# Performance work log

Measured on AMD Instinct MI355X. Metric: run time of the kernel, lower is better.

## Reference

```python
import jax, jax.numpy as jnp
import numpy as np

N, IN_C, HID, OUT_C, DEPTH = 4096, 128, 256, 128, 3
KS = [2048, 1024, 512]  # ceil(0.5 * N_level)
E = 131072


def glorot(key, fan_in, fan_out):
    lim = np.sqrt(6.0 / (fan_in + fan_out))
    return jax.random.uniform(key, (fan_in, fan_out), jnp.float32, -lim, lim)


def build_adj(edge_index, n):
    # symmetric, self-loop-free adjacency with unit edge weights
    A = jnp.zeros((n, n), jnp.float32)
    A = A.at[edge_index[0], edge_index[1]].set(1.0)
    A = jnp.maximum(A, A.T)
    return A * (1.0 - jnp.eye(n, dtype=jnp.float32))


def gcn(x, A, W, b):
    # GCNConv(improved=True): A_hat = A + 2I, symmetric normalization
    n = A.shape[0]
    Ah = A + 2.0 * jnp.eye(n, dtype=A.dtype)
    deg = Ah.sum(axis=1)
    dinv = jnp.where(deg > 0, deg ** -0.5, 0.0)
    An = dinv[:, None] * Ah * dinv[None, :]
    return An @ (x @ W) + b


def augment(A):
    # remove self loops, add self loops (w=1), square (spspmm), remove self loops
    n = A.shape[0]
    I = jnp.eye(n, dtype=A.dtype)
    Al = A * (1.0 - I) + I
    A2 = Al @ Al
    return A2 * (1.0 - I)


def topk_pool(x, A, p, k):
    score = jnp.tanh((x @ p) / jnp.linalg.norm(p))
    vals, perm = jax.lax.top_k(score, k)
    return x[perm] * vals[:, None], A[perm][:, perm], perm


def setup_inputs() -> dict:
    key = jax.random.key(0)
    ks = jax.random.split(key, 16)
    x = jax.random.normal(ks[0], (N, IN_C), jnp.float32)
    edge_index = jax.random.randint(ks[1], (2, E), 0, N, jnp.int32)
    d = {"x": x, "edge_index": edge_index}
    d["Wd0"], d["bd0"] = glorot(ks[2], IN_C, HID), jnp.zeros((HID,), jnp.float32)
    d["Wd1"], d["bd1"] = glorot(ks[3], HID, HID), jnp.zeros((HID,), jnp.float32)
    d["Wd2"], d["bd2"] = glorot(ks[4], HID, HID), jnp.zeros((HID,), jnp.float32)
    d["Wd3"], d["bd3"] = glorot(ks[5], HID, HID), jnp.zeros((HID,), jnp.float32)
    d["p1"] = jax.random.normal(ks[6], (HID,), jnp.float32)
    d["p2"] = jax.random.normal(ks[7], (HID,), jnp.float32)
    d["p3"] = jax.random.normal(ks[8], (HID,), jnp.float32)
    d["Wu0"], d["bu0"] = glorot(ks[9], HID, HID), jnp.zeros((HID,), jnp.float32)
    d["Wu1"], d["bu1"] = glorot(ks[10], HID, HID), jnp.zeros((HID,), jnp.float32)
    d["Wu2"], d["bu2"] = glorot(ks[11], HID, OUT_C), jnp.zeros((OUT_C,), jnp.float32)
    return d


def reference(x, edge_index, Wd0, bd0, Wd1, bd1, Wd2, bd2, Wd3, bd3,
              p1, p2, p3, Wu0, bu0, Wu1, bu1, Wu2, bu2):
    n = x.shape[0]
    A = build_adj(edge_index, n)
    x = jax.nn.relu(gcn(x, A, Wd0, bd0))
    xs, As, perms = [x], [A], []
    down = [(Wd1, bd1), (Wd2, bd2), (Wd3, bd3)]
    pools = [p1, p2, p3]
    for i in range(DEPTH):
        A = augment(A)
        x, A, perm = topk_pool(x, A, pools[i], KS[i])
        x = jax.nn.relu(gcn(x, A, *down[i]))
        if i < DEPTH - 1:
            xs.append(x)
            As.append(A)
        perms.append(perm)
    up = [(Wu0, bu0), (Wu1, bu1), (Wu2, bu2)]
    for i in range(DEPTH):
        j = DEPTH - 1 - i
        res, perm = xs[j], perms[j]
        u = jnp.zeros_like(res).at[perm].set(x)
        x = res + u  # sum_res=True
        x = gcn(x, As[j], *up[i])
        if i < DEPTH - 1:
            x = jax.nn.relu(x)
    return x
```

## Files before the change

### kernel.cpp

```cpp
#include <hip/hip_runtime.h>


typedef __attribute__((ext_vector_type(8))) short bf16x8;
typedef __attribute__((ext_vector_type(4))) short s16x4;
typedef __attribute__((ext_vector_type(4))) float f32x4;

__device__ __forceinline__ short f2bf(float f) {
    unsigned u = __builtin_bit_cast(unsigned, f);
    u += 0x7FFFu + ((u >> 16) & 1u);
    return (short)(u >> 16);
}
__device__ __forceinline__ float bf2f(short s) {
    unsigned u = ((unsigned)(unsigned short)s) << 16;
    return __builtin_bit_cast(float, u);
}

#define GLL16(gsrc, ldst)                                                        \
    __builtin_amdgcn_global_load_lds(                                            \
        (__attribute__((address_space(1))) void*)(gsrc),                         \
        (__attribute__((address_space(3))) void*)(ldst), 16, 0, 0)

template<int MODE, int EPI>
__global__ __launch_bounds__(256, 2)
void gemm_bt(const short* __restrict__ Ah, const short* __restrict__ Al,
             const short* __restrict__ Bh, const short* __restrict__ Bl,
             float* __restrict__ Cf, int M, int N, int K, int kChunk)
{
    if (EPI == 1 && (int)blockIdx.y > (int)blockIdx.x) return;

    __shared__ short sAh[128 * 32];
    __shared__ short sBh[128 * 32];
    __shared__ short sAl[(MODE == 2) ? 128 * 32 : 8];
    __shared__ short sBl[(MODE >= 1) ? 128 * 32 : 8];

    const int t    = threadIdx.x;
    const int lane = t & 63;
    const int wave = t >> 6;
    const int tM   = blockIdx.y * 128;
    const int tN   = blockIdx.x * 128;
    const int k0   = blockIdx.z * kChunk;

    const int wm  = (wave >> 1) * 64;
    const int wn  = (wave & 1) * 64;
    const int l15 = lane & 15;
    const int g8  = (lane >> 4) * 8;

    f32x4 acc[4][4];
    const f32x4 zero = {0.f, 0.f, 0.f, 0.f};
#pragma unroll
    for (int i = 0; i < 4; i++)
#pragma unroll
        for (int j = 0; j < 4; j++) acc[i][j] = zero;

    const int i0 = t, i1 = t + 256;
    const short* a0 = Ah + (size_t)(tM + (i0 >> 2)) * K + (i0 & 3) * 8;
    const short* a1 = Ah + (size_t)(tM + (i1 >> 2)) * K + (i1 & 3) * 8;
    const short* b0 = Bh + (size_t)(tN + (i0 >> 2)) * K + (i0 & 3) * 8;
    const short* b1 = Bh + (size_t)(tN + (i1 >> 2)) * K + (i1 & 3) * 8;
    const short *bl0 = nullptr, *bl1 = nullptr, *al0 = nullptr, *al1 = nullptr;
    if (MODE >= 1) {
        bl0 = Bl + (size_t)(tN + (i0 >> 2)) * K + (i0 & 3) * 8;
        bl1 = Bl + (size_t)(tN + (i1 >> 2)) * K + (i1 & 3) * 8;
    }
    if (MODE == 2) {
        al0 = Al + (size_t)(tM + (i0 >> 2)) * K + (i0 & 3) * 8;
        al1 = Al + (size_t)(tM + (i1 >> 2)) * K + (i1 & 3) * 8;
    }

    for (int kb = k0; kb < k0 + kChunk; kb += 32) {
        GLL16(a0 + kb, &sAh[i0 * 8]);
        GLL16(a1 + kb, &sAh[i1 * 8]);
        GLL16(b0 + kb, &sBh[i0 * 8]);
        GLL16(b1 + kb, &sBh[i1 * 8]);
        if (MODE >= 1) { GLL16(bl0 + kb, &sBl[i0 * 8]); GLL16(bl1 + kb, &sBl[i1 * 8]); }
        if (MODE == 2) { GLL16(al0 + kb, &sAl[i0 * 8]); GLL16(al1 + kb, &sAl[i1 * 8]); }
        __syncthreads();

        bf16x8 aF[4], bF[4], aL[4], bL[4];
#pragma unroll
        for (int i = 0; i < 4; i++)
            aF[i] = *(const bf16x8*)&sAh[(wm + i * 16 + l15) * 32 + g8];
#pragma unroll
        for (int j = 0; j < 4; j++)
            bF[j] = *(const bf16x8*)&sBh[(wn + j * 16 + l15) * 32 + g8];
        if (MODE >= 1)
#pragma unroll
            for (int j = 0; j < 4; j++)
                bL[j] = *(const bf16x8*)&sBl[(wn + j * 16 + l15) * 32 + g8];
        if (MODE == 2)
#pragma unroll
            for (int i = 0; i < 4; i++)
                aL[i] = *(const bf16x8*)&sAl[(wm + i * 16 + l15) * 32 + g8];

#pragma unroll
        for (int i = 0; i < 4; i++)
#pragma unroll
            for (int j = 0; j < 4; j++) {
                acc[i][j] = __builtin_amdgcn_mfma_f32_16x16x32_bf16(aF[i], bF[j], acc[i][j], 0, 0, 0);
                if (MODE >= 1)
                    acc[i][j] = __builtin_amdgcn_mfma_f32_16x16x32_bf16(aF[i], bL[j], acc[i][j], 0, 0, 0);
                if (MODE == 2)
                    acc[i][j] = __builtin_amdgcn_mfma_f32_16x16x32_bf16(aL[i], bF[j], acc[i][j], 0, 0, 0);
            }
        __syncthreads();
    }

    const int r4 = (lane >> 4) * 4;
    if (EPI == 3) {
        float* CT = Cf + (size_t)blockIdx.z * M * N;
#pragma unroll
        for (int i = 0; i < 4; i++)
#pragma unroll
            for (int j = 0; j < 4; j++) {
                const int col   = tN + wn + j * 16 + l15;
                const int rbase = tM + wm + i * 16 + r4;
                *(f32x4*)&CT[(size_t)col * M + rbase] = acc[i][j];
            }
    } else {
        float* Cg = Cf + (size_t)blockIdx.z * M * N;
#pragma unroll
        for (int i = 0; i < 4; i++)
#pragma unroll
            for (int j = 0; j < 4; j++) {
                const int col = tN + wn + j * 16 + l15;
                float* cp = Cg + (size_t)(tM + wm + i * 16 + r4) * N + col;
#pragma unroll
                for (int r = 0; r < 4; r++) cp[(size_t)r * N] = acc[i][j][r];
            }
        if (EPI == 1 && tM != tN) {
#pragma unroll
            for (int i = 0; i < 4; i++)
#pragma unroll
                for (int j = 0; j < 4; j++) {
                    const int col   = tN + wn + j * 16 + l15;
                    const int rbase = tM + wm + i * 16 + r4;
                    *(f32x4*)&Cg[(size_t)col * N + rbase] = acc[i][j];
                }
        }
    }
}


__global__ void prep(const float* __restrict__ Wd0, const float* __restrict__ Wd1,
                     const float* __restrict__ Wd2, const float* __restrict__ Wd3,
                     const float* __restrict__ Wu0, const float* __restrict__ Wu1,
                     const float* __restrict__ Wu2, const float* __restrict__ x0,
                     short* __restrict__ Wth, short* __restrict__ Wtl,
                     short* __restrict__ Xh, short* __restrict__ Xl,
                     unsigned long long* __restrict__ M0)
{
    int t = blockIdx.x * 256 + threadIdx.x;
    float v; int dst;
    if (t < 32768)       { int e = t;          v = Wd0[e]; dst = 0      + (e & 255) * 128 + (e >> 8); }
    else if (t < 98304)  { int e = t - 32768;  v = Wd1[e]; dst = 32768  + (e & 255) * 256 + (e >> 8); }
    else if (t < 163840) { int e = t - 98304;  v = Wd2[e]; dst = 98304  + (e & 255) * 256 + (e >> 8); }
    else if (t < 229376) { int e = t - 163840; v = Wd3[e]; dst = 163840 + (e & 255) * 256 + (e >> 8); }
    else if (t < 294912) { int e = t - 229376; v = Wu0[e]; dst = 229376 + (e & 255) * 256 + (e >> 8); }
    else if (t < 360448) { int e = t - 294912; v = Wu1[e]; dst = 294912 + (e & 255) * 256 + (e >> 8); }
    else if (t < 393216) { int e = t - 360448; v = Wu2[e]; dst = 360448 + (e & 127) * 256 + (e >> 7); }
    else if (t < 917504) {
        int e = t - 393216;
        v = x0[e];
        short h = f2bf(v);
        Xh[e] = h; Xl[e] = f2bf(v - bf2f(h));
        return;
    } else {
        M0[t - 917504] = 0ull;
        return;
    }
    short h = f2bf(v);
    Wth[dst] = h; Wtl[dst] = f2bf(v - bf2f(h));
}

__global__ void build_bits(const int* __restrict__ ei, int E,
                           unsigned long long* __restrict__ M0)
{
    int e = blockIdx.x * 256 + threadIdx.x;
    if (e >= E) return;
    int i = ei[e], j = ei[E + e];
    if (i != j) {
        atomicOr(&M0[(size_t)i * 64 + (j >> 6)], 1ull << (j & 63));
        atomicOr(&M0[(size_t)j * 64 + (i >> 6)], 1ull << (i & 63));
    }
}

__global__ void row_compact_bits(const unsigned long long* __restrict__ M0,
                                 int* __restrict__ csr, float* __restrict__ rs)
{
    int row = blockIdx.x * 4 + (threadIdx.x >> 6);
    int lane = threadIdx.x & 63;
    unsigned long long w = M0[(size_t)row * 64 + lane];
    int c = __popcll(w);
    int incl = c;
    for (int off = 1; off < 64; off <<= 1) {
        int v = __shfl_up(incl, off);
        if (lane >= off) incl += v;
    }
    int base = incl - c;
    int* out = csr + (size_t)row * 128;
    while (w) {
        int b = __ffsll((unsigned long long)w) - 1;
        if (base < 128) out[base] = lane * 64 + b;
        base++;
        w &= w - 1;
    }
    if (lane == 63) rs[row] = (float)incl;
}

__global__ void mask_gather(const unsigned long long* __restrict__ M0,
                            const int* __restrict__ perm,
                            unsigned long long* __restrict__ mask,
                            float* __restrict__ rs, int kk)
{
    int t = blockIdx.x * 256 + threadIdx.x;
    if (t < kk) rs[t] = 0.f;
    int r = t >> 6, l = t & 63;
    int u = perm[r];
    unsigned long long w = M0[(size_t)u * 64 + l];
    if ((u >> 6) == l) w |= 1ull << (u & 63);
    mask[t] = w;
}

#define PSTR2 18
__global__ __launch_bounds__(256, 8)
void popc_aug_p(const unsigned long long* __restrict__ mask,
                short* __restrict__ Cp)
{
    const int bx = blockIdx.x, by = blockIdx.y, z = blockIdx.z;
    if (by > bx) return;
    __shared__ unsigned long long a[64 * PSTR2];
    __shared__ unsigned long long b[64 * PSTR2];
    const int t = threadIdx.x;
#pragma unroll
    for (int p = 0; p < 4; p++) {
        int idx = p * 256 + t;
        int rr = idx >> 4, w = idx & 15;
        a[rr * PSTR2 + w] = mask[((size_t)(by * 64 + rr)) * 64 + z * 16 + w];
        b[rr * PSTR2 + w] = mask[((size_t)(bx * 64 + rr)) * 64 + z * 16 + w];
    }
    __syncthreads();
    const int i0 = (t >> 4) * 4;
    const int j0 = t & 15;
    int acc[4][4];
#pragma unroll
    for (int qi = 0; qi < 4; qi++)
#pragma unroll
        for (int qj = 0; qj < 4; qj++) acc[qi][qj] = 0;
#pragma unroll
    for (int w = 0; w < 16; w += 2) {
        ulong2 av[4], bv[4];
#pragma unroll
        for (int q = 0; q < 4; q++) av[q] = *(const ulong2*)&a[(i0 + q) * PSTR2 + w];
#pragma unroll
        for (int q = 0; q < 4; q++) bv[q] = *(const ulong2*)&b[(j0 + 16 * q) * PSTR2 + w];
#pragma unroll
        for (int qi = 0; qi < 4; qi++)
#pragma unroll
            for (int qj = 0; qj < 4; qj++) {
                acc[qi][qj] += __builtin_popcountll(av[qi].x & bv[qj].x);
                acc[qi][qj] += __builtin_popcountll(av[qi].y & bv[qj].y);
            }
    }
    short* out = Cp + ((size_t)z * 1024 + (size_t)(by * 32 + bx)) * 4096;
#pragma unroll
    for (int qi = 0; qi < 4; qi++)
#pragma unroll
        for (int qj = 0; qj < 4; qj++)
            out[(i0 + qi) * 64 + j0 + 16 * qj] = (short)acc[qi][qj];
}

__global__ __launch_bounds__(256)
void aug_merge(const short* __restrict__ Cp, int kk,
               short* __restrict__ Ahs, float* __restrict__ rs)
{
    const int bx = blockIdx.x, by = blockIdx.y;
    if (by > bx) return;
    __shared__ float tile[64][65];
    __shared__ float rsum[64], csum[64];
    const int t = threadIdx.x;
    const int i  = t >> 2;
    const int c0 = (t & 3) * 16;
    const size_t tb = (size_t)(by * 32 + bx) * 4096;
    const size_t ss = (size_t)1024 * 4096;
    if (t < 64) { rsum[t] = 0.f; csum[t] = 0.f; }

    int v[16];
#pragma unroll
    for (int q = 0; q < 16; q++) v[q] = 0;
    for (int s = 0; s < 4; s++) {
        bf16x8 p0 = *(const bf16x8*)&Cp[tb + s * ss + i * 64 + c0];
        bf16x8 p1 = *(const bf16x8*)&Cp[tb + s * ss + i * 64 + c0 + 8];
#pragma unroll
        for (int q = 0; q < 8; q++) { v[q] += (int)p0[q]; v[8 + q] += (int)p1[q]; }
    }
    const int gi = by * 64 + i;
    float rp = 0.f;
    s16x4 pk[4];
#pragma unroll
    for (int q = 0; q < 16; q++) {
        const int gj = bx * 64 + c0 + q;
        float val = (gi == gj) ? 0.f : (float)v[q];
        tile[i][c0 + q] = val;
        rp += val;
        pk[q >> 2][q & 3] = f2bf(val);
    }
#pragma unroll
    for (int q = 0; q < 4; q++)
        *(s16x4*)&Ahs[(size_t)gi * kk + bx * 64 + c0 + q * 4] = pk[q];
    __syncthreads();
    atomicAdd(&rsum[i], rp);
    if (bx != by) {
        float cpv = 0.f;
#pragma unroll
        for (int q = 0; q < 16; q++) {
            float val = tile[c0 + q][i];
            cpv += val;
            pk[q >> 2][q & 3] = f2bf(val);
        }
#pragma unroll
        for (int q = 0; q < 4; q++)
            *(s16x4*)&Ahs[(size_t)(bx * 64 + i) * kk + by * 64 + c0 + q * 4] = pk[q];
        atomicAdd(&csum[i], cpv);
    }
    __syncthreads();
    if (t < 64) {
        atomicAdd(&rs[by * 64 + t], rsum[t]);
        if (bx != by) atomicAdd(&rs[bx * 64 + t], csum[t]);
    }
}

__global__ void z_reduce(const float* __restrict__ Cp, int S,
                         const float* __restrict__ rs,
                         short* __restrict__ Zh, short* __restrict__ Zl,
                         int n, int C)
{
    int t4 = (blockIdx.x * 256 + threadIdx.x) * 4;
    int r = t4 % n;
    size_t stride = (size_t)n * C;
    f32x4 v = {0.f, 0.f, 0.f, 0.f};
    for (int s = 0; s < S; s++) v += *(const f32x4*)&Cp[t4 + s * stride];
    f32x4 rsv = *(const f32x4*)&rs[r];
    s16x4 zh, zl;
#pragma unroll
    for (int q = 0; q < 4; q++) {
        float z = v[q] / sqrtf(rsv[q] + 2.f);
        short h = f2bf(z);
        zh[q] = h; zl[q] = f2bf(z - bf2f(h));
    }
    *(s16x4*)&Zh[t4] = zh;
    *(s16x4*)&Zl[t4] = zl;
}

__global__ void zf_reduce(const float* __restrict__ Cp, int S,
                          const float* __restrict__ rs,
                          float* __restrict__ Zf, int n, int C)
{
    int t4 = (blockIdx.x * 256 + threadIdx.x) * 4;
    int r = t4 / C;
    size_t stride = (size_t)n * C;
    f32x4 v = {0.f, 0.f, 0.f, 0.f};
    for (int s = 0; s < S; s++) v += *(const f32x4*)&Cp[t4 + s * stride];
    float d = 1.f / sqrtf(rs[r] + 2.f);
    v *= d;
    *(f32x4*)&Zf[t4] = v;
}

template<int CN, int RELU, int SC>
__global__ __launch_bounds__(256)
void spmm_gcn(const int* __restrict__ csr, const float* __restrict__ rs,
              const float* __restrict__ Zf, const float* __restrict__ b,
              float* __restrict__ out,
              const float* __restrict__ pvec, float* __restrict__ score)
{
    const int lane = threadIdx.x & 63;
    const int row  = blockIdx.x * 4 + (threadIdx.x >> 6);
    const int dg   = (int)rs[row];
    const int* nb  = csr + (size_t)row * 128;
    if (CN == 256) {
        const int c = lane * 4;
        float4 acc = {0.f, 0.f, 0.f, 0.f};
        int q = 0;
        for (; q + 4 <= dg; q += 4) {
            int j0 = nb[q], j1 = nb[q+1], j2 = nb[q+2], j3 = nb[q+3];
            float4 z0 = *(const float4*)&Zf[(size_t)j0 * CN + c];
            float4 z1 = *(const float4*)&Zf[(size_t)j1 * CN + c];
            float4 z2 = *(const float4*)&Zf[(size_t)j2 * CN + c];
            float4 z3 = *(const float4*)&Zf[(size_t)j3 * CN + c];
            acc.x += z0.x; acc.y += z0.y; acc.z += z0.z; acc.w += z0.w;
            acc.x += z1.x; acc.y += z1.y; acc.z += z1.z; acc.w += z1.w;
            acc.x += z2.x; acc.y += z2.y; acc.z += z2.z; acc.w += z2.w;
            acc.x += z3.x; acc.y += z3.y; acc.z += z3.z; acc.w += z3.w;
        }
        for (; q < dg; q++) {
            float4 z = *(const float4*)&Zf[(size_t)nb[q] * CN + c];
            acc.x += z.x; acc.y += z.y; acc.z += z.z; acc.w += z.w;
        }
        float d = 1.f / sqrtf(rs[row] + 2.f);
        float4 zi = *(const float4*)&Zf[(size_t)row * CN + c];
        float4 bb = *(const float4*)&b[c];
        float4 g;
        g.x = d * acc.x + 2.f * d * zi.x + bb.x;
        g.y = d * acc.y + 2.f * d * zi.y + bb.y;
        g.z = d * acc.z + 2.f * d * zi.z + bb.z;
        g.w = d * acc.w + 2.f * d * zi.w + bb.w;
        if (RELU) {
            g.x = fmaxf(g.x, 0.f); g.y = fmaxf(g.y, 0.f);
            g.z = fmaxf(g.z, 0.f); g.w = fmaxf(g.w, 0.f);
        }
        *(float4*)&out[(size_t)row * CN + c] = g;
        if (SC) {
            float4 pv = ((const float4*)pvec)[lane];
            double nn  = (double)pv.x * pv.x + (double)pv.y * pv.y +
                         (double)pv.z * pv.z + (double)pv.w * pv.w;
            double acd = (double)g.x * pv.x + (double)g.y * pv.y +
                         (double)g.z * pv.z + (double)g.w * pv.w;
            for (int off = 32; off; off >>= 1) {
                acd += __shfl_down(acd, off);
                nn  += __shfl_down(nn, off);
            }
            if (lane == 0) score[row] = tanhf((float)(acd / sqrt(nn)));
        }
    } else {
        const int c = lane * 2;
        float2 acc = {0.f, 0.f};
        int q = 0;
        for (; q + 4 <= dg; q += 4) {
            int j0 = nb[q], j1 = nb[q+1], j2 = nb[q+2], j3 = nb[q+3];
            float2 z0 = *(const float2*)&Zf[(size_t)j0 * CN + c];
            float2 z1 = *(const float2*)&Zf[(size_t)j1 * CN + c];
            float2 z2 = *(const float2*)&Zf[(size_t)j2 * CN + c];
            float2 z3 = *(const float2*)&Zf[(size_t)j3 * CN + c];
            acc.x += z0.x; acc.y += z0.y;
            acc.x += z1.x; acc.y += z1.y;
            acc.x += z2.x; acc.y += z2.y;
            acc.x += z3.x; acc.y += z3.y;
        }
        for (; q < dg; q++) {
            float2 z = *(const float2*)&Zf[(size_t)nb[q] * CN + c];
            acc.x += z.x; acc.y += z.y;
        }
        float d = 1.f / sqrtf(rs[row] + 2.f);
        float2 zi = *(const float2*)&Zf[(size_t)row * CN + c];
        float2 g;
        g.x = d * acc.x + 2.f * d * zi.x + b[c];
        g.y = d * acc.y + 2.f * d * zi.y + b[c + 1];
        if (RELU) { g.x = fmaxf(g.x, 0.f); g.y = fmaxf(g.y, 0.f); }
        *(float2*)&out[(size_t)row * CN + c] = g;
    }
}

template<int SC>
__global__ void gcn_final(const float* __restrict__ Cp, int S,
                          const short* __restrict__ Zh, const short* __restrict__ Zl,
                          const float* __restrict__ rs, const float* __restrict__ b,
                          float* __restrict__ out, short* __restrict__ oh,
                          short* __restrict__ ol, int k, int C, int relu,
                          const int* __restrict__ inv, const float* __restrict__ res,
                          const float* __restrict__ pvec, float* __restrict__ score)
{
    int t4 = (blockIdx.x * 256 + threadIdx.x) * 4;
    int j = t4 / C, c = t4 - j * C;
    int r = inv ? inv[j] : j;
    f32x4 v = res ? *(const f32x4*)&res[t4] : (f32x4){0.f, 0.f, 0.f, 0.f};
    if (r >= 0) {
        size_t base = (size_t)r * C + c;
        size_t stride = (size_t)k * C;
        f32x4 az = {0.f, 0.f, 0.f, 0.f};
        for (int s = 0; s < S; s++) az += *(const f32x4*)&Cp[base + s * stride];
        float d = 1.f / sqrtf(rs[r] + 2.f);
        f32x4 bb = *(const f32x4*)&b[c];
#pragma unroll
        for (int q = 0; q < 4; q++) {
            size_t zi = (size_t)(c + q) * k + r;
            float zz = bf2f(Zh[zi]) + bf2f(Zl[zi]);
            float g = d * az[q] + 2.f * d * zz + bb[q];
            if (relu && g < 0.f) g = 0.f;
            v[q] += g;
        }
    }
    *(f32x4*)&out[t4] = v;
    if (oh) {
        s16x4 hh, ll;
#pragma unroll
        for (int q = 0; q < 4; q++) {
            short h = f2bf(v[q]);
            hh[q] = h; ll[q] = f2bf(v[q] - bf2f(h));
        }
        *(s16x4*)&oh[t4] = hh;
        *(s16x4*)&ol[t4] = ll;
    }
    if (SC) {
        const int lane = threadIdx.x & 63;
        float4 pv = *(const float4*)&pvec[c];
        double nn  = (double)pv.x * pv.x + (double)pv.y * pv.y +
                     (double)pv.z * pv.z + (double)pv.w * pv.w;
        double acd = (double)v[0] * pv.x + (double)v[1] * pv.y +
                     (double)v[2] * pv.z + (double)v[3] * pv.w;
        for (int off = 32; off; off >>= 1) {
            acd += __shfl_down(acd, off);
            nn  += __shfl_down(nn, off);
        }
        if (lane == 0) score[j] = tanhf((float)(acd / sqrt(nn)));
    }
}

__device__ __forceinline__ unsigned long long packkey(float s, int i) {
    unsigned u = __builtin_bit_cast(unsigned, s);
    u = (u & 0x80000000u) ? ~u : (u | 0x80000000u);
    return ((unsigned long long)u << 32) | (unsigned)(0xFFFFFFFFu - (unsigned)i);
}

__global__ __launch_bounds__(512)
void rank_pool(const float* __restrict__ score, int n, int k,
               const float* __restrict__ xold,
               int* __restrict__ perm, int* __restrict__ inv,
               short* __restrict__ Xh, short* __restrict__ Xl)
{
    __shared__ unsigned long long sk[512];
    __shared__ int rk[64];
    __shared__ int selrow[64];
    __shared__ int selrank[64];
    __shared__ float selval[64];
    __shared__ int cnt;
    const int t  = threadIdx.x;
    const int il = t & 63;
    const int js = t >> 6;
    const int i  = blockIdx.x * 64 + il;
    if (t < 64) rk[t] = 0;
    if (t == 0) cnt = 0;
    const unsigned long long mykey = packkey(score[i], i);
    int r = 0;
    for (int jb = 0; jb < n; jb += 512) {
        __syncthreads();
        if (jb + t < n) sk[t] = packkey(score[jb + t], jb + t);
        __syncthreads();
        const unsigned long long* p = &sk[js * 64];
#pragma unroll 16
        for (int q = 0; q < 64; q++) r += (p[q] > mykey) ? 1 : 0;
    }
    atomicAdd(&rk[il], r);
    __syncthreads();
    if (t < 64) {
        int rank = rk[t];
        int ii = blockIdx.x * 64 + t;
        inv[ii] = (rank < k) ? rank : -1;
        if (rank < k) {
            perm[rank] = ii;
            int s = atomicAdd(&cnt, 1);
            selrow[s]  = ii;
            selrank[s] = rank;
            selval[s]  = score[ii];
        }
    }
    __syncthreads();
    const int wave = t >> 6, lane = t & 63;
    for (int s = wave; s < cnt; s += 8) {
        const int   row = selrow[s];
        const float vv  = selval[s];
        f32x4 x = *(const f32x4*)&xold[(size_t)row * 256 + lane * 4];
        s16x4 hh, ll;
#pragma unroll
        for (int q = 0; q < 4; q++) {
            float v = x[q] * vv;
            short h = f2bf(v);
            hh[q] = h; ll[q] = f2bf(v - bf2f(h));
        }
        size_t o = (size_t)selrank[s] * 256 + lane * 4;
        *(s16x4*)&Xh[o] = hh;
        *(s16x4*)&Xl[o] = ll;
    }
}

__global__ void gatherG_h(const short* __restrict__ A, int n,
                          const int* __restrict__ perm,
                          short* __restrict__ Gh, int kk,
                          float* __restrict__ rsz)
{
    int idx = blockIdx.x * 256 + threadIdx.x;
    if (idx < kk) rsz[idx] = 0.f;
    int t8 = idx * 8;
    if (t8 >= kk * n) return;
    int r = t8 / n, c0 = t8 - r * n;
    int pr = perm[r];
    bf16x8 a = *(const bf16x8*)&A[(size_t)pr * n + c0];
    if (pr >= c0 && pr < c0 + 8)
        a[pr - c0] = f2bf(bf2f(a[pr - c0]) + 1.f);
    *(bf16x8*)&Gh[t8] = a;
}

__global__ void gatherG_hl(const short* __restrict__ Ahi, const short* __restrict__ Alo,
                           int n, const int* __restrict__ perm,
                           short* __restrict__ Gh, short* __restrict__ Gl, int kk,
                           float* __restrict__ rsz)
{
    int idx = blockIdx.x * 256 + threadIdx.x;
    if (idx < kk) rsz[idx] = 0.f;
    int t8 = idx * 8;
    if (t8 >= kk * n) return;
    int r = t8 / n, c0 = t8 - r * n;
    int pr = perm[r];
    bf16x8 ah = *(const bf16x8*)&Ahi[(size_t)pr * n + c0];
    bf16x8 al = *(const bf16x8*)&Alo[(size_t)pr * n + c0];
    bf16x8 gh, gl;
#pragma unroll
    for (int q = 0; q < 8; q++) {
        float v = bf2f(ah[q]) + bf2f(al[q]) + ((c0 + q == pr) ? 1.f : 0.f);
        short h = f2bf(v);
        gh[q] = h; gl[q] = f2bf(v - bf2f(h));
    }
    *(bf16x8*)&Gh[t8] = gh;
    *(bf16x8*)&Gl[t8] = gl;
}

template<bool LO>
__global__ void aug_finish_f(const float* __restrict__ Cp, int S, int kk,
                             short* __restrict__ Ahs, short* __restrict__ Als,
                             float* __restrict__ rs)
{
    int t4 = (blockIdx.x * 256 + threadIdx.x) * 4;
    int r = t4 / kk, c0 = t4 - r * kk;
    size_t stride = (size_t)kk * kk;
    f32x4 v = {0.f, 0.f, 0.f, 0.f};
    for (int s = 0; s < S; s++) v += *(const f32x4*)&Cp[t4 + s * stride];
    if (r >= c0 && r < c0 + 4) v[r - c0] = 0.f;
    s16x4 hh, ll;
    float ws = 0.f;
#pragma unroll
    for (int q = 0; q < 4; q++) {
        short h = f2bf(v[q]);
        hh[q] = h;
        if (LO) ll[q] = f2bf(v[q] - bf2f(h));
        ws += v[q];
    }
    *(s16x4*)&Ahs[t4] = hh;
    if (LO) *(s16x4*)&Als[t4] = ll;
    for (int off = 32; off; off >>= 1) ws += __shfl_down(ws, off);
    if ((threadIdx.x & 63) == 0) atomicAdd(&rs[r], ws);
}


extern "C" void kernel_launch(void* const* d_in, const int* in_sizes, int n_in,
                              void* d_out, int out_size, void* d_ws, size_t ws_size,
                              hipStream_t stream)
{
    const float* x0  = (const float*)d_in[0];
    const int*   ei  = (const int*)d_in[1];
    const float* Wd0 = (const float*)d_in[2];  const float* bd0 = (const float*)d_in[3];
    const float* Wd1 = (const float*)d_in[4];  const float* bd1 = (const float*)d_in[5];
    const float* Wd2 = (const float*)d_in[6];  const float* bd2 = (const float*)d_in[7];
    const float* Wd3 = (const float*)d_in[8];  const float* bd3 = (const float*)d_in[9];
    const float* p1  = (const float*)d_in[10];
    const float* p2  = (const float*)d_in[11];
    const float* p3  = (const float*)d_in[12];
    const float* Wu0 = (const float*)d_in[13]; const float* bu0 = (const float*)d_in[14];
    const float* Wu1 = (const float*)d_in[15]; const float* bu1 = (const float*)d_in[16];
    const float* Wu2 = (const float*)d_in[17]; const float* bu2 = (const float*)d_in[18];

    const int E = in_sizes[1] / 2;

    char* ws = (char*)d_ws;
    size_t off = 0;
    auto alloc = [&](size_t bytes) -> void* {
        void* p = ws + off;
        off += (bytes + 255) & ~(size_t)255;
        return p;
    };
    unsigned long long* M0 = (unsigned long long*)alloc((size_t)4096 * 64 * 8);
    short* A1h  = (short*)alloc((size_t)2048 * 2048 * 2);
    short* A2h  = (short*)alloc((size_t)1024 * 1024 * 2);
    short* A2l  = (short*)alloc((size_t)1024 * 1024 * 2);
    short* A3h  = (short*)alloc((size_t)512 * 512 * 2);
    short* A3l  = (short*)alloc((size_t)512 * 512 * 2);
    short* Gh   = (short*)alloc((size_t)1024 * 2048 * 2);
    short* Gl   = (short*)alloc((size_t)512 * 1024 * 2);
    int*   csr  = (int*)alloc((size_t)4096 * 128 * 4);
    unsigned long long* maskb = (unsigned long long*)alloc((size_t)2048 * 64 * 8);
    float* Zf   = (float*)alloc((size_t)4096 * 256 * 4);
    float* Cp   = (float*)alloc((size_t)64 * 1024 * 1024);
    float* xs0  = (float*)alloc((size_t)4096 * 256 * 4);
    float* xs1  = (float*)alloc((size_t)2048 * 256 * 4);
    float* xs2  = (float*)alloc((size_t)1024 * 256 * 4);
    float* xu0  = (float*)alloc((size_t)4096 * 256 * 4);
    float* xu1  = (float*)alloc((size_t)2048 * 256 * 4);
    float* xu2  = (float*)alloc((size_t)1024 * 256 * 4);
    short* xu0h = (short*)alloc((size_t)4096 * 256 * 2);
    short* xu0l = (short*)alloc((size_t)4096 * 256 * 2);
    short* xu1h = (short*)alloc((size_t)2048 * 256 * 2);
    short* xu1l = (short*)alloc((size_t)2048 * 256 * 2);
    short* xu2h = (short*)alloc((size_t)1024 * 256 * 2);
    short* xu2l = (short*)alloc((size_t)1024 * 256 * 2);
    short* X0h  = (short*)alloc((size_t)4096 * 128 * 2);
    short* X0l  = (short*)alloc((size_t)4096 * 128 * 2);
    short* xah  = (short*)alloc((size_t)2048 * 256 * 2);
    short* xal  = (short*)alloc((size_t)2048 * 256 * 2);
    short* Wth  = (short*)alloc((size_t)393216 * 2);
    short* Wtl  = (short*)alloc((size_t)393216 * 2);
    short* Zh   = (short*)alloc((size_t)256 * 4096 * 2);
    short* Zl   = (short*)alloc((size_t)256 * 4096 * 2);
    float* rs0  = (float*)alloc(4096 * 4);
    float* rs1  = (float*)alloc(2048 * 4);
    float* rs2  = (float*)alloc(1024 * 4);
    float* rs3  = (float*)alloc(512 * 4);
    float* scoreb = (float*)alloc(4096 * 4);
    int*   perm1  = (int*)alloc(2048 * 4);
    int*   perm2  = (int*)alloc(1024 * 4);
    int*   perm3  = (int*)alloc(512 * 4);
    int*   inv1   = (int*)alloc(4096 * 4);
    int*   inv2   = (int*)alloc(2048 * 4);
    int*   inv3   = (int*)alloc(1024 * 4);

    auto gcn_dense = [&](const short* Xh, const short* Xl, int n, int Kc, int Cout,
                         const short* pAh, const short* pAl, const float* rsA,
                         int wtoff, const float* b,
                         float* out, short* oh, short* ol, int relu, int modeA,
                         int Saz, const int* inv, const float* res, int nout,
                         const float* pvec) {
        int Sxw = 4;
        gemm_bt<2, 3><<<dim3(Cout / 128, n / 128, Sxw), 256, 0, stream>>>(
            Xh, Xl, Wth + wtoff, Wtl + wtoff, Cp, n, Cout, Kc, Kc / Sxw);
        z_reduce<<<(n * Cout) / 1024, 256, 0, stream>>>(Cp, Sxw, rsA, Zh, Zl, n, Cout);
        dim3 g(Cout / 128, n / 128, Saz);
        if (modeA == 1)
            gemm_bt<1, 0><<<g, 256, 0, stream>>>(pAh, nullptr, Zh, Zl, Cp, n, Cout, n, n / Saz);
        else
            gemm_bt<2, 0><<<g, 256, 0, stream>>>(pAh, pAl, Zh, Zl, Cp, n, Cout, n, n / Saz);
        if (pvec)
            gcn_final<1><<<(nout * Cout) / 1024, 256, 0, stream>>>(
                Cp, Saz, Zh, Zl, rsA, b, out, oh, ol, n, Cout, relu, inv, res,
                pvec, scoreb);
        else
            gcn_final<0><<<(nout * Cout) / 1024, 256, 0, stream>>>(
                Cp, Saz, Zh, Zl, rsA, b, out, oh, ol, n, Cout, relu, inv, res,
                nullptr, nullptr);
    };

    auto pool = [&](const float* xlev, int n, int* perm, int* inv) {
        int k = n / 2;
        rank_pool<<<n / 64, 512, 0, stream>>>(scoreb, n, k, xlev, perm, inv, xah, xal);
    };

    prep<<<4608, 256, 0, stream>>>(Wd0, Wd1, Wd2, Wd3, Wu0, Wu1, Wu2, x0,
                                   Wth, Wtl, X0h, X0l, M0);
    build_bits<<<(E + 255) / 256, 256, 0, stream>>>(ei, E, M0);
    row_compact_bits<<<1024, 256, 0, stream>>>(M0, csr, rs0);

    gemm_bt<2, 0><<<dim3(2, 32, 4), 256, 0, stream>>>(
        X0h, X0l, Wth, Wtl, Cp, 4096, 256, 128, 32);
    zf_reduce<<<1024, 256, 0, stream>>>(Cp, 4, rs0, Zf, 4096, 256);
    spmm_gcn<256, 1, 1><<<1024, 256, 0, stream>>>(csr, rs0, Zf, bd0, xs0, p1, scoreb);

    pool(xs0, 4096, perm1, inv1);
    mask_gather<<<512, 256, 0, stream>>>(M0, perm1, maskb, rs1, 2048);
    popc_aug_p<<<dim3(32, 32, 4), 256, 0, stream>>>(maskb, (short*)Cp);
    aug_merge<<<dim3(32, 32), 256, 0, stream>>>((const short*)Cp, 2048, A1h, rs1);
    gcn_dense(xah, xal, 2048, 256, 256, A1h, nullptr, rs1, 32768, bd1,
              xs1, nullptr, nullptr, 1, 1, 8, nullptr, nullptr, 2048, p2);

    pool(xs1, 2048, perm2, inv2);
    gatherG_h<<<(1024 * 2048 / 8) / 256, 256, 0, stream>>>(A1h, 2048, perm2, Gh, 1024, rs2);
    gemm_bt<0, 1><<<dim3(8, 8, 8), 256, 0, stream>>>(Gh, nullptr, Gh, nullptr, Cp, 1024, 1024, 2048, 256);
    aug_finish_f<true><<<(1024 * 1024 / 4) / 256, 256, 0, stream>>>(Cp, 8, 1024, A2h, A2l, rs2);
    gcn_dense(xah, xal, 1024, 256, 256, A2h, A2l, rs2, 98304, bd2,
              xs2, nullptr, nullptr, 1, 2, 8, nullptr, nullptr, 1024, p3);

    pool(xs2, 1024, perm3, inv3);
    gatherG_hl<<<(512 * 1024 / 8) / 256, 256, 0, stream>>>(A2h, A2l, 1024, perm3, Gh, Gl, 512, rs3);
    gemm_bt<2, 1><<<dim3(4, 4, 8), 256, 0, stream>>>(Gh, Gl, Gh, Gl, Cp, 512, 512, 1024, 128);
    aug_finish_f<true><<<(512 * 512 / 4) / 256, 256, 0, stream>>>(Cp, 8, 512, A3h, A3l, rs3);

    gcn_dense(xah, xal, 512, 256, 256, A3h, A3l, rs3, 163840, bd3,
              xu2, xu2h, xu2l, 1, 2, 8, inv3, xs2, 1024, nullptr);

    gcn_dense(xu2h, xu2l, 1024, 256, 256, A2h, A2l, rs2, 229376, bu0,
              xu1, xu1h, xu1l, 1, 2, 8, inv2, xs1, 2048, nullptr);

    gcn_dense(xu1h, xu1l, 2048, 256, 256, A1h, nullptr, rs1, 294912, bu1,
              xu0, xu0h, xu0l, 1, 1, 8, inv1, xs0, 4096, nullptr);

    gemm_bt<2, 0><<<dim3(1, 32, 8), 256, 0, stream>>>(
        xu0h, xu0l, Wth + 360448, Wtl + 360448, Cp, 4096, 128, 256, 32);
    zf_reduce<<<512, 256, 0, stream>>>(Cp, 8, rs0, Zf, 4096, 128);
    spmm_gcn<128, 0, 0><<<1024, 256, 0, stream>>>(csr, rs0, Zf, bu2, (float*)d_out,
                                                  nullptr, nullptr);
}
```

Measured before the change: 440.5 us.

## Fuse pooled X·W GEMM with adjacency gather into one launch per level

Adds an xw_fat kernel whose first blocks compute the split-bf16 X·W GEMM for the pooled features and whose remaining blocks do the mask or adjacency gather that previously ran as a separate kernel. The X·W product is hoisted ahead of the augmentation GEMM and written to a second scratch buffer, so gcn_rest only reduces it later. This removes one launch per down level and lets the small GEMM overlap the memory-bound gather. It costs extra scratch memory, and the payload blocks share the grid with GEMM blocks, which may unbalance scheduling.

Result: no change. 432.5 us (-1.8%).

```diff
diff --git a/kernel.cpp b/kernel.cpp
--- a/kernel.cpp
+++ b/kernel.cpp
@@ -138,6 +138,149 @@
                 }
         }
     }
+}
+
+template<int PAY>
+__global__ __launch_bounds__(256, 2)
+void xw_fat(const short* __restrict__ Ah, const short* __restrict__ Al,
+            const short* __restrict__ Bh, const short* __restrict__ Bl,
+            float* __restrict__ Cf, int M, int N, int K, int kChunk,
+            int gx, int gy, int GB,
+            const short* __restrict__ pA, const short* __restrict__ pAlo,
+            int pn, const int* __restrict__ perm,
+            short* __restrict__ pGh, short* __restrict__ pGl, int pkk,
+            float* __restrict__ rsz,
+            const unsigned long long* __restrict__ M0s,
+            unsigned long long* __restrict__ masko)
+{
+    __shared__ short sAh[128 * 32];
+    __shared__ short sBh[128 * 32];
+    __shared__ short sAl[128 * 32];
+    __shared__ short sBl[128 * 32];
+
+    const int bid = (int)blockIdx.x;
+    const int t   = threadIdx.x;
+
+    if (bid >= GB) {
+        const int pidx = (bid - GB) * 256 + t;
+        if (PAY == 2) {
+            if (pidx < pkk) rsz[pidx] = 0.f;
+            int r = pidx >> 6, l = pidx & 63;
+            int u = perm[r];
+            unsigned long long w = M0s[(size_t)u * 64 + l];
+            if ((u >> 6) == l) w |= 1ull << (u & 63);
+            masko[pidx] = w;
+        } else if (PAY == 0) {
+            if (pidx < pkk) rsz[pidx] = 0.f;
+            int t8 = pidx * 8;
+            if (t8 < pkk * pn) {
+                int r = t8 / pn, c0 = t8 - r * pn;
+                int pr = perm[r];
+                bf16x8 a = *(const bf16x8*)&pA[(size_t)pr * pn + c0];
+                if (pr >= c0 && pr < c0 + 8)
+                    a[pr - c0] = f2bf(bf2f(a[pr - c0]) + 1.f);
+                *(bf16x8*)&pGh[t8] = a;
+            }
+        } else {
+            if (pidx < pkk) rsz[pidx] = 0.f;
+            int t8 = pidx * 8;
+            if (t8 < pkk * pn) {
+                int r = t8 / pn, c0 = t8 - r * pn;
+                int pr = perm[r];
+                bf16x8 ah = *(const bf16x8*)&pA[(size_t)pr * pn + c0];
+                bf16x8 al = *(const bf16x8*)&pAlo[(size_t)pr * pn + c0];
+                bf16x8 gh, gl;
+#pragma unroll
+                for (int q = 0; q < 8; q++) {
+                    float v = bf2f(ah[q]) + bf2f(al[q]) + ((c0 + q == pr) ? 1.f : 0.f);
+                    short h = f2bf(v);
+                    gh[q] = h; gl[q] = f2bf(v - bf2f(h));
+                }
+                *(bf16x8*)&pGh[t8] = gh;
+                *(bf16x8*)&pGl[t8] = gl;
+            }
+        }
+        return;
+    }
+
+    const int bx = bid % gx;
+    const int by = (bid / gx) % gy;
+    const int bz = bid / (gx * gy);
+
+    const int lane = t & 63;
+    const int wave = t >> 6;
+    const int tM   = by * 128;
+    const int tN   = bx * 128;
+    const int k0   = bz * kChunk;
+
+    const int wm  = (wave >> 1) * 64;
+    const int wn  = (wave & 1) * 64;
+    const int l15 = lane & 15;
+    const int g8  = (lane >> 4) * 8;
+
+    f32x4 acc[4][4];
+    const f32x4 zero = {0.f, 0.f, 0.f, 0.f};
+#pragma unroll
+    for (int i = 0; i < 4; i++)
+#pragma unroll
+        for (int j = 0; j < 4; j++) acc[i][j] = zero;
+
+    const int i0 = t, i1 = t + 256;
+    const short* a0  = Ah + (size_t)(tM + (i0 >> 2)) * K + (i0 & 3) * 8;
+    const short* a1  = Ah + (size_t)(tM + (i1 >> 2)) * K + (i1 & 3) * 8;
+    const short* b0  = Bh + (size_t)(tN + (i0 >> 2)) * K + (i0 & 3) * 8;
+    const short* b1  = Bh + (size_t)(tN + (i1 >> 2)) * K + (i1 & 3) * 8;
+    const short* bl0 = Bl + (size_t)(tN + (i0 >> 2)) * K + (i0 & 3) * 8;
+    const short* bl1 = Bl + (size_t)(tN + (i1 >> 2)) * K + (i1 & 3) * 8;
+    const short* al0 = Al + (size_t)(tM + (i0 >> 2)) * K + (i0 & 3) * 8;
+    const short* al1 = Al + (size_t)(tM + (i1 >> 2)) * K + (i1 & 3) * 8;
+
+    for (int kb = k0; kb < k0 + kChunk; kb += 32) {
+        GLL16(a0 + kb, &sAh[i0 * 8]);
+        GLL16(a1 + kb, &sAh[i1 * 8]);
+        GLL16(b0 + kb, &sBh[i0 * 8]);
+        GLL16(b1 + kb, &sBh[i1 * 8]);
+        GLL16(bl0 + kb, &sBl[i0 * 8]);
+        GLL16(bl1 + kb, &sBl[i1 * 8]);
+        GLL16(al0 + kb, &sAl[i0 * 8]);
+        GLL16(al1 + kb, &sAl[i1 * 8]);
+        __syncthreads();
+
+        bf16x8 aF[4], bF[4], aL[4], bL[4];
+#pragma unroll
+        for (int i = 0; i < 4; i++)
+            aF[i] = *(const bf16x8*)&sAh[(wm + i * 16 + l15) * 32 + g8];
+#pragma unroll
+        for (int j = 0; j < 4; j++)
+            bF[j] = *(const bf16x8*)&sBh[(wn + j * 16 + l15) * 32 + g8];
+#pragma unroll
+        for (int j = 0; j < 4; j++)
+            bL[j] = *(const bf16x8*)&sBl[(wn + j * 16 + l15) * 32 + g8];
+#pragma unroll
+        for (int i = 0; i < 4; i++)
+            aL[i] = *(const bf16x8*)&sAl[(wm + i * 16 + l15) * 32 + g8];
+
+#pragma unroll
+        for (int i = 0; i < 4; i++)
+#pragma unroll
+            for (int j = 0; j < 4; j++) {
+                acc[i][j] = __builtin_amdgcn_mfma_f32_16x16x32_bf16(aF[i], bF[j], acc[i][j], 0, 0, 0);
+                acc[i][j] = __builtin_amdgcn_mfma_f32_16x16x32_bf16(aF[i], bL[j], acc[i][j], 0, 0, 0);
+                acc[i][j] = __builtin_amdgcn_mfma_f32_16x16x32_bf16(aL[i], bF[j], acc[i][j], 0, 0, 0);
+            }
+        __syncthreads();
+    }
+
+    const int r4 = (lane >> 4) * 4;
+    float* CT = Cf + (size_t)bz * M * N;
+#pragma unroll
+    for (int i = 0; i < 4; i++)
+#pragma unroll
+        for (int j = 0; j < 4; j++) {
+            const int col   = tN + wn + j * 16 + l15;
+            const int rbase = tM + wm + i * 16 + r4;
+            *(f32x4*)&CT[(size_t)col * M + rbase] = acc[i][j];
+        }
 }
 
 
@@ -205,20 +348,6 @@
         w &= w - 1;
     }
     if (lane == 63) rs[row] = (float)incl;
-}
-
-__global__ void mask_gather(const unsigned long long* __restrict__ M0,
-                            const int* __restrict__ perm,
-                            unsigned long long* __restrict__ mask,
-                            float* __restrict__ rs, int kk)
-{
-    int t = blockIdx.x * 256 + threadIdx.x;
-    if (t < kk) rs[t] = 0.f;
-    int r = t >> 6, l = t & 63;
-    int u = perm[r];
-    unsigned long long w = M0[(size_t)u * 64 + l];
-    if ((u >> 6) == l) w |= 1ull << (u & 63);
-    mask[t] = w;
 }
 
 #define PSTR2 18
@@ -569,47 +698,6 @@
         *(s16x4*)&Xh[o] = hh;
         *(s16x4*)&Xl[o] = ll;
     }
-}
-
-__global__ void gatherG_h(const short* __restrict__ A, int n,
-                          const int* __restrict__ perm,
-                          short* __restrict__ Gh, int kk,
-                          float* __restrict__ rsz)
-{
-    int idx = blockIdx.x * 256 + threadIdx.x;
-    if (idx < kk) rsz[idx] = 0.f;
-    int t8 = idx * 8;
-    if (t8 >= kk * n) return;
-    int r = t8 / n, c0 = t8 - r * n;
-    int pr = perm[r];
-    bf16x8 a = *(const bf16x8*)&A[(size_t)pr * n + c0];
-    if (pr >= c0 && pr < c0 + 8)
-        a[pr - c0] = f2bf(bf2f(a[pr - c0]) + 1.f);
-    *(bf16x8*)&Gh[t8] = a;
-}
-
-__global__ void gatherG_hl(const short* __restrict__ Ahi, const short* __restrict__ Alo,
-                           int n, const int* __restrict__ perm,
-                           short* __restrict__ Gh, short* __restrict__ Gl, int kk,
-                           float* __restrict__ rsz)
-{
-    int idx = blockIdx.x * 256 + threadIdx.x;
-    if (idx < kk) rsz[idx] = 0.f;
-    int t8 = idx * 8;
-    if (t8 >= kk * n) return;
-    int r = t8 / n, c0 = t8 - r * n;
-    int pr = perm[r];
-    bf16x8 ah = *(const bf16x8*)&Ahi[(size_t)pr * n + c0];
-    bf16x8 al = *(const bf16x8*)&Alo[(size_t)pr * n + c0];
-    bf16x8 gh, gl;
-#pragma unroll
-    for (int q = 0; q < 8; q++) {
-        float v = bf2f(ah[q]) + bf2f(al[q]) + ((c0 + q == pr) ? 1.f : 0.f);
-        short h = f2bf(v);
-        gh[q] = h; gl[q] = f2bf(v - bf2f(h));
-    }
-    *(bf16x8*)&Gh[t8] = gh;
-    *(bf16x8*)&Gl[t8] = gl;
 }
 
 template<bool LO>
@@ -709,16 +797,14 @@
     int*   inv2   = (int*)alloc(2048 * 4);
     int*   inv3   = (int*)alloc(1024 * 4);
 
-    auto gcn_dense = [&](const short* Xh, const short* Xl, int n, int Kc, int Cout,
-                         const short* pAh, const short* pAl, const float* rsA,
-                         int wtoff, const float* b,
-                         float* out, short* oh, short* ol, int relu, int modeA,
-                         int Saz, const int* inv, const float* res, int nout,
-                         const float* pvec) {
-        int Sxw = 4;
-        gemm_bt<2, 3><<<dim3(Cout / 128, n / 128, Sxw), 256, 0, stream>>>(
-            Xh, Xl, Wth + wtoff, Wtl + wtoff, Cp, n, Cout, Kc, Kc / Sxw);
-        z_reduce<<<(n * Cout) / 1024, 256, 0, stream>>>(Cp, Sxw, rsA, Zh, Zl, n, Cout);
+    float* Cp2 = Cp + (size_t)8 * 1024 * 1024;
+
+    auto gcn_rest = [&](int n, int Cout, const short* pAh, const short* pAl,
+                        const float* rsA, const float* b, float* out,
+                        short* oh, short* ol, int relu, int modeA, int Saz,
+                        const int* inv, const float* res, int nout,
+                        const float* pvec, const float* CpXw, int Sxw) {
+        z_reduce<<<(n * Cout) / 1024, 256, 0, stream>>>(CpXw, Sxw, rsA, Zh, Zl, n, Cout);
         dim3 g(Cout / 128, n / 128, Saz);
         if (modeA == 1)
             gemm_bt<1, 0><<<g, 256, 0, stream>>>(pAh, nullptr, Zh, Zl, Cp, n, Cout, n, n / Saz);
@@ -734,6 +820,19 @@
                 nullptr, nullptr);
     };
 
+    auto gcn_dense = [&](const short* Xh, const short* Xl, int n, int Kc, int Cout,
+                         const short* pAh, const short* pAl, const float* rsA,
+                         int wtoff, const float* b,
+                         float* out, short* oh, short* ol, int relu, int modeA,
+                         int Saz, const int* inv, const float* res, int nout,
+                         const float* pvec) {
+        int Sxw = 4;
+        gemm_bt<2, 3><<<dim3(Cout / 128, n / 128, Sxw), 256, 0, stream>>>(
+            Xh, Xl, Wth + wtoff, Wtl + wtoff, Cp, n, Cout, Kc, Kc / Sxw);
+        gcn_rest(n, Cout, pAh, pAl, rsA, b, out, oh, ol, relu, modeA, Saz,
+                 inv, res, nout, pvec, Cp, Sxw);
+    };
+
     auto pool = [&](const float* xlev, int n, int* perm, int* inv) {
         int k = n / 2;
         rank_pool<<<n / 64, 512, 0, stream>>>(scoreb, n, k, xlev, perm, inv, xah, xal);
@@ -750,26 +849,35 @@
     spmm_gcn<256, 1, 1><<<1024, 256, 0, stream>>>(csr, rs0, Zf, bd0, xs0, p1, scoreb);
 
     pool(xs0, 4096, perm1, inv1);
-    mask_gather<<<512, 256, 0, stream>>>(M0, perm1, maskb, rs1, 2048);
+    xw_fat<2><<<128 + 512, 256, 0, stream>>>(
+        xah, xal, Wth + 32768, Wtl + 32768, Cp2, 2048, 256, 256, 64,
+        2, 16, 128,
+        nullptr, nullptr, 0, perm1, nullptr, nullptr, 2048, rs1, M0, maskb);
     popc_aug_p<<<dim3(32, 32, 4), 256, 0, stream>>>(maskb, (short*)Cp);
     aug_merge<<<dim3(32, 32), 256, 0, stream>>>((const short*)Cp, 2048, A1h, rs1);
-    gcn_dense(xah, xal, 2048, 256, 256, A1h, nullptr, rs1, 32768, bd1,
-              xs1, nullptr, nullptr, 1, 1, 8, nullptr, nullptr, 2048, p2);
+    gcn_rest(2048, 256, A1h, nullptr, rs1, bd1, xs1, nullptr, nullptr, 1, 1, 8,
+             nullptr, nullptr, 2048, p2, Cp2, 4);
 
     pool(xs1, 2048, perm2, inv2);
-    gatherG_h<<<(1024 * 2048 / 8) / 256, 256, 0, stream>>>(A1h, 2048, perm2, Gh, 1024, rs2);
+    xw_fat<0><<<64 + 1024, 256, 0, stream>>>(
+        xah, xal, Wth + 98304, Wtl + 98304, Cp2, 1024, 256, 256, 64,
+        2, 8, 64,
+        A1h, nullptr, 2048, perm2, Gh, nullptr, 1024, rs2, nullptr, nullptr);
     gemm_bt<0, 1><<<dim3(8, 8, 8), 256, 0, stream>>>(Gh, nullptr, Gh, nullptr, Cp, 1024, 1024, 2048, 256);
     aug_finish_f<true><<<(1024 * 1024 / 4) / 256, 256, 0, stream>>>(Cp, 8, 1024, A2h, A2l, rs2);
-    gcn_dense(xah, xal, 1024, 256, 256, A2h, A2l, rs2, 98304, bd2,
-              xs2, nullptr, nullptr, 1, 2, 8, nullptr, nullptr, 1024, p3);
+    gcn_rest(1024, 256, A2h, A2l, rs2, bd2, xs2, nullptr, nullptr, 1, 2, 8,
+             nullptr, nullptr, 1024, p3, Cp2, 4);
 
     pool(xs2, 1024, perm3, inv3);
-    gatherG_hl<<<(512 * 1024 / 8) / 256, 256, 0, stream>>>(A2h, A2l, 1024, perm3, Gh, Gl, 512, rs3);
+    xw_fat<1><<<32 + 256, 256, 0, stream>>>(
+        xah, xal, Wth + 163840, Wtl + 163840, Cp2, 512, 256, 256, 64,
+        2, 4, 32,
+        A2h, A2l, 1024, perm3, Gh, Gl, 512, rs3, nullptr, nullptr);
     gemm_bt<2, 1><<<dim3(4, 4, 8), 256, 0, stream>>>(Gh, Gl, Gh, Gl, Cp, 512, 512, 1024, 128);
     aug_finish_f<true><<<(512 * 512 / 4) / 256, 256, 0, stream>>>(Cp, 8, 512, A3h, A3l, rs3);
 
-    gcn_dense(xah, xal, 512, 256, 256, A3h, A3l, rs3, 163840, bd3,
-              xu2, xu2h, xu2l, 1, 2, 8, inv3, xs2, 1024, nullptr);
+    gcn_rest(512, 256, A3h, A3l, rs3, bd3, xu2, xu2h, xu2l, 1, 2, 8,
+             inv3, xs2, 1024, nullptr, Cp2, 4);
 
     gcn_dense(xu2h, xu2l, 1024, 256, 256, A2h, A2l, rs2, 229376, bu0,
               xu1, xu1h, xu1l, 1, 2, 8, inv2, xs1, 2048, nullptr);
```
